# Kernel tuning notes

Measured on AMD Instinct MI355X. Metric: run time of the kernel, lower is better.

Reference implementation:

```python
import jax, jax.numpy as jnp
import numpy as np

QLEN, BSZ, D_MODEL = 1024, 4, 1024
N_HEAD, D_HEAD = 16, 64
RLEN = QLEN  # rlen == klen -> classic _rel_shift path
LN_EPS = 1e-5


def setup_inputs() -> dict:
    key = jax.random.key(0)
    ks = jax.random.split(key, 9)
    s = 0.02
    w = jax.random.normal(ks[0], (QLEN, BSZ, D_MODEL), jnp.float32)
    r = jax.random.normal(ks[1], (RLEN, D_MODEL), jnp.float32)
    # causal mask: True = masked (future positions)
    attn_mask = jnp.triu(jnp.ones((QLEN, QLEN), jnp.bool_), k=1)
    qkv_w = jax.random.normal(ks[2], (D_MODEL, 3 * N_HEAD * D_HEAD), jnp.float32) * s
    r_w = jax.random.normal(ks[3], (D_MODEL, N_HEAD * D_HEAD), jnp.float32) * s
    o_w = jax.random.normal(ks[4], (N_HEAD * D_HEAD, D_MODEL), jnp.float32) * s
    r_r_bias = jax.random.normal(ks[5], (N_HEAD, D_HEAD), jnp.float32) * s
    r_w_bias = jax.random.normal(ks[6], (N_HEAD, D_HEAD), jnp.float32) * s
    ln_g = jnp.ones((D_MODEL,), jnp.float32)
    ln_b = jnp.zeros((D_MODEL,), jnp.float32)
    return {"w": w, "r": r, "attn_mask": attn_mask, "qkv_w": qkv_w,
            "r_w": r_w, "o_w": o_w, "r_r_bias": r_r_bias,
            "r_w_bias": r_w_bias, "ln_g": ln_g, "ln_b": ln_b}


def _rel_shift(x):
    # x: [qlen, klen, bsz, n_head] -> Transformer-XL relative shift
    q, k, b, n = x.shape
    zero_pad = jnp.zeros((q, 1, b, n), x.dtype)
    x_padded = jnp.concatenate([zero_pad, x], axis=1)      # [q, k+1, b, n]
    x_padded = x_padded.reshape(k + 1, q, b, n)
    return x_padded[1:].reshape(q, k, b, n)


def _layer_norm(x, g, b):
    mu = jnp.mean(x, axis=-1, keepdims=True)
    var = jnp.mean(jnp.square(x - mu), axis=-1, keepdims=True)
    return (x - mu) * jax.lax.rsqrt(var + LN_EPS) * g + b


def reference(w, r, attn_mask, qkv_w, r_w, o_w, r_r_bias, r_w_bias, ln_g, ln_b):
    qlen, bsz, _ = w.shape
    H, D = r_r_bias.shape
    scale = 1.0 / D ** 0.5

    w_heads = w @ qkv_w                                    # [q, b, 3*H*D]
    q_h, k_h, v_h = jnp.split(w_heads, 3, axis=-1)
    q_h = q_h.reshape(qlen, bsz, H, D)
    k_h = k_h.reshape(qlen, bsz, H, D)
    v_h = v_h.reshape(qlen, bsz, H, D)
    r_k = (r @ r_w).reshape(-1, H, D)                      # [rlen, H, D]

    AC = jnp.einsum('ibnd,jbnd->ijbn', q_h + r_w_bias, k_h)
    BD = _rel_shift(jnp.einsum('ibnd,jnd->ijbn', q_h + r_r_bias, r_k))
    score = (AC + BD) * scale                              # [q, k, b, n]
    score = jnp.where(attn_mask[:, :, None, None], -1e30, score)

    prob = jax.nn.softmax(score, axis=1)
    vec = jnp.einsum('ijbn,jbnd->ibnd', prob, v_h).reshape(qlen, bsz, H * D)
    attn_out = vec @ o_w
    return _layer_norm(w + attn_out, ln_g, ln_b)
```

## Files before the change

### kernel.cpp

```cpp
#include <hip/hip_runtime.h>
#include <hip/hip_bf16.h>

#define SEQ    1024
#define BSZW   4
#define DMODEL 1024
#define NHEAD  16
#define DHEAD  64
#define MROWS  (SEQ*BSZW)
#define QKVN   (3*NHEAD*DHEAD)

typedef __attribute__((ext_vector_type(8))) short short8;
typedef __attribute__((ext_vector_type(4))) float f32x4;

__device__ __forceinline__ float bf2f(short s) {
    union { int i; float f; } u; u.i = ((int)(unsigned short)s) << 16; return u.f;
}
__device__ __forceinline__ short f2bf(float f) {
    union { float f; unsigned int u; } v; v.f = f;
    unsigned int r = v.u + 0x7FFFu + ((v.u >> 16) & 1u);
    return (short)(unsigned short)(r >> 16);
}

__device__ __forceinline__ void async16(const void* g, void* s) {
    __builtin_amdgcn_global_load_lds(
        (__attribute__((address_space(1))) void*)(g),
        (__attribute__((address_space(3))) void*)(s), 16, 0, 0);
}

__global__ __launch_bounds__(256) void prep_all(const float* __restrict__ w,
                                                const float* __restrict__ r,
                                                const float* __restrict__ qkv_w,
                                                const float* __restrict__ r_w,
                                                const float* __restrict__ o_w,
                                                short* __restrict__ Wb,
                                                short* __restrict__ rb,
                                                short* __restrict__ QKVt,
                                                short* __restrict__ RWt,
                                                short* __restrict__ OWt)
{
    const int z = blockIdx.z;
    const int tid = threadIdx.x;
    if (z == 3) {
        size_t flat = (size_t)blockIdx.y * 96 + blockIdx.x;
        if (flat >= 2560) return;
        size_t idx = flat * 2048 + (size_t)tid * 8;
        const float* in = w; short* out = Wb;
        if (idx >= (size_t)4194304) { in = r; out = rb; idx -= 4194304; }
        float4 a = *(const float4*)(in + idx);
        float4 b = *(const float4*)(in + idx + 4);
        out[idx + 0] = f2bf(a.x); out[idx + 1] = f2bf(a.y);
        out[idx + 2] = f2bf(a.z); out[idx + 3] = f2bf(a.w);
        out[idx + 4] = f2bf(b.x); out[idx + 5] = f2bf(b.y);
        out[idx + 6] = f2bf(b.z); out[idx + 7] = f2bf(b.w);
        return;
    }
    const int bx = blockIdx.x, by = blockIdx.y;
    const float* in; short* out; int C;
    if (z == 0)      { in = qkv_w; out = QKVt; C = QKVN; }
    else if (z == 1) { in = r_w;   out = RWt;  C = DMODEL; if (bx >= 32) return; }
    else             { in = o_w;   out = OWt;  C = DMODEL; if (bx >= 32) return; }
    const int R = DMODEL;
    __shared__ short t[32][33];
    const int rr0 = tid >> 5, c = tid & 31;
    #pragma unroll
    for (int rr = 0; rr < 4; ++rr) {
        int rl = rr0 + rr * 8;
        t[c][rl] = f2bf(in[(size_t)(by * 32 + rl) * C + bx * 32 + c]);
    }
    __syncthreads();
    #pragma unroll
    for (int rr = 0; rr < 4; ++rr) {
        int rl = rr0 + rr * 8;
        out[(size_t)(bx * 32 + rl) * R + by * 32 + c] = t[rl][c];
    }
}

__global__ __launch_bounds__(256) void vtrans(const short* __restrict__ in,
                                              short* __restrict__ out)
{
    __shared__ short t[32][33];
    const int tid = threadIdx.x;
    const int r = tid >> 5, c = tid & 31;
    const int bx = blockIdx.x, by = blockIdx.y, bh = blockIdx.z;
    #pragma unroll
    for (int rr = 0; rr < 4; ++rr) {
        int rl = r + rr * 8;
        t[c][rl] = in[((size_t)bh * SEQ + bx * 32 + rl) * DHEAD + by * 32 + c];
    }
    __syncthreads();
    #pragma unroll
    for (int rr = 0; rr < 4; ++rr) {
        int rl = r + rr * 8;
        out[((size_t)bh * DHEAD + by * 32 + rl) * SEQ + bx * 32 + c] = t[rl][c];
    }
}

#define GEMM_BODY_128(A_, Bt_, K_)                                             \
    __shared__ short As[128 * 32];                                              \
    __shared__ short Bs[128 * 32];                                              \
    const int w = tid >> 6, lane = tid & 63;                                    \
    const int L15 = lane & 15, quad = lane >> 4;                                \
    const int mq = (w & 1) * 64, nq = (w >> 1) * 64;                            \
    f32x4 acc[4][4];                                                            \
    _Pragma("unroll")                                                           \
    for (int i = 0; i < 4; ++i)                                                 \
        _Pragma("unroll")                                                       \
        for (int j = 0; j < 4; ++j) acc[i][j] = (f32x4){0.f, 0.f, 0.f, 0.f};    \
    const int srow  = w * 16 + (lane >> 2);                                     \
    const int schnk = ((lane & 3) ^ (lane >> 4)) * 8;                           \
    const int rpA = (quad ^ (L15 >> 2)) * 8;                                    \
    for (int k0 = 0; k0 < K_; k0 += 32) {                                       \
        __syncthreads();                                                        \
        _Pragma("unroll")                                                       \
        for (int q = 0; q < 2; ++q) {                                           \
            async16(A_ + (size_t)(m0 + q * 64 + srow) * K_ + k0 + schnk,        \
                    &As[(q * 64 + w * 16) * 32]);                               \
            async16(Bt_ + (size_t)(n0 + q * 64 + srow) * K_ + k0 + schnk,       \
                    &Bs[(q * 64 + w * 16) * 32]);                               \
        }                                                                       \
        __syncthreads();                                                        \
        short8 a[4], b[4];                                                      \
        _Pragma("unroll")                                                       \
        for (int rt = 0; rt < 4; ++rt)                                          \
            a[rt] = *(const short8*)&As[(mq + rt * 16 + L15) * 32 + rpA];       \
        _Pragma("unroll")                                                       \
        for (int ct = 0; ct < 4; ++ct)                                          \
            b[ct] = *(const short8*)&Bs[(nq + ct * 16 + L15) * 32 + rpA];       \
        _Pragma("unroll")                                                       \
        for (int rt = 0; rt < 4; ++rt)                                          \
            _Pragma("unroll")                                                   \
            for (int ct = 0; ct < 4; ++ct)                                      \
                acc[rt][ct] = __builtin_amdgcn_mfma_f32_16x16x32_bf16(          \
                    a[rt], b[ct], acc[rt][ct], 0, 0, 0);                        \
    }

__global__ __launch_bounds__(256) void qkv_rk_mfma(const short* __restrict__ Wb,
                                                   const short* __restrict__ QKVt,
                                                   const short* __restrict__ rbuf,
                                                   const short* __restrict__ RWt,
                                                   const float* __restrict__ rwb,
                                                   const float* __restrict__ rrb,
                                                   short* __restrict__ Qwb,
                                                   short* __restrict__ Qrb,
                                                   short* __restrict__ Kb,
                                                   short* __restrict__ Vb,
                                                   short* __restrict__ RK)
{
    const int tid = threadIdx.x;
    const int by = blockIdx.y;
    const bool isrk = (by >= 32);
    if (isrk && blockIdx.x >= 8) return;
    const short* A_  = isrk ? rbuf : Wb;
    const short* Bt_ = isrk ? RWt : QKVt;
    const int m0 = (isrk ? (by - 32) : by) * 128;
    const int n0 = blockIdx.x * 128;
    GEMM_BODY_128(A_, Bt_, 1024)

    if (isrk) {
        const int h = (n0 + nq) >> 6;
        #pragma unroll
        for (int rt = 0; rt < 4; ++rt)
            #pragma unroll
            for (int g = 0; g < 4; ++g) {
                int m = m0 + mq + rt * 16 + quad * 4 + g;
                #pragma unroll
                for (int ct = 0; ct < 4; ++ct)
                    RK[((size_t)h * SEQ + m) * DHEAD + ct * 16 + L15] =
                        f2bf(acc[rt][ct][g]);
            }
        return;
    }
    const int nb = n0 + nq;
    const int chunk = nb >> 10;
    const int h = (nb >> 6) & 15;
    float rw4[4], rr4[4];
    if (chunk == 0) {
        #pragma unroll
        for (int ct = 0; ct < 4; ++ct) {
            rw4[ct] = rwb[h * DHEAD + ct * 16 + L15];
            rr4[ct] = rrb[h * DHEAD + ct * 16 + L15];
        }
    }
    #pragma unroll
    for (int rt = 0; rt < 4; ++rt)
        #pragma unroll
        for (int g = 0; g < 4; ++g) {
            int m = m0 + mq + rt * 16 + quad * 4 + g;
            int qi = m >> 2, b = m & 3;
            size_t rowbase = ((size_t)(b * NHEAD + h) * SEQ + qi) * DHEAD;
            #pragma unroll
            for (int ct = 0; ct < 4; ++ct) {
                int d = ct * 16 + L15;
                float v = acc[rt][ct][g];
                if (chunk == 0) {
                    Qwb[rowbase + d] = f2bf(v + rw4[ct]);
                    Qrb[rowbase + d] = f2bf(v + rr4[ct]);
                } else if (chunk == 1) {
                    Kb[rowbase + d] = f2bf(v);
                } else {
                    Vb[rowbase + d] = f2bf(v);
                }
            }
        }
}

__global__ __launch_bounds__(256) void oproj_mfma(const short* __restrict__ A,
                                                  const short* __restrict__ Bt,
                                                  float* __restrict__ C)
{
    __shared__ short As[128 * 32];
    __shared__ short Bs[64 * 32];
    const int tid = threadIdx.x;
    const int w = tid >> 6, lane = tid & 63;
    const int L15 = lane & 15, quad = lane >> 4;
    const int n0 = blockIdx.x * 64, m0 = blockIdx.y * 128;
    const int mq = w * 32;
    f32x4 acc[2][4];
    #pragma unroll
    for (int i = 0; i < 2; ++i)
        #pragma unroll
        for (int j = 0; j < 4; ++j) acc[i][j] = (f32x4){0.f, 0.f, 0.f, 0.f};
    const int srow  = w * 16 + (lane >> 2);
    const int schnk = ((lane & 3) ^ (lane >> 4)) * 8;
    const int rpA = (quad ^ (L15 >> 2)) * 8;
    for (int k0 = 0; k0 < 1024; k0 += 32) {
        __syncthreads();
        #pragma unroll
        for (int q = 0; q < 2; ++q)
            async16(A + (size_t)(m0 + q * 64 + srow) * 1024 + k0 + schnk,
                    &As[(q * 64 + w * 16) * 32]);
        async16(Bt + (size_t)(n0 + srow) * 1024 + k0 + schnk, &Bs[(w * 16) * 32]);
        __syncthreads();
        short8 a[2], b[4];
        #pragma unroll
        for (int rt = 0; rt < 2; ++rt)
            a[rt] = *(const short8*)&As[(mq + rt * 16 + L15) * 32 + rpA];
        #pragma unroll
        for (int ct = 0; ct < 4; ++ct)
            b[ct] = *(const short8*)&Bs[(ct * 16 + L15) * 32 + rpA];
        #pragma unroll
        for (int rt = 0; rt < 2; ++rt)
            #pragma unroll
            for (int ct = 0; ct < 4; ++ct)
                acc[rt][ct] = __builtin_amdgcn_mfma_f32_16x16x32_bf16(
                    a[rt], b[ct], acc[rt][ct], 0, 0, 0);
    }
    #pragma unroll
    for (int rt = 0; rt < 2; ++rt)
        #pragma unroll
        for (int g = 0; g < 4; ++g) {
            int m = m0 + mq + rt * 16 + quad * 4 + g;
            #pragma unroll
            for (int ct = 0; ct < 4; ++ct)
                C[(size_t)m * DMODEL + n0 + ct * 16 + L15] = acc[rt][ct][g];
        }
}

__global__ __launch_bounds__(256) void attn_mfma(const short* __restrict__ Qw,
                                                 const short* __restrict__ Qr,
                                                 const short* __restrict__ Kg,
                                                 const short* __restrict__ Vt,
                                                 const short* __restrict__ RK,
                                                 short* __restrict__ ATT)
{
    __shared__ short Ks[2][64 * 64];
    __shared__ short Vts[2][64 * 64];
    __shared__ short Pbuf[4][16][136];

    const int tid  = threadIdx.x;
    const int w    = tid >> 6;
    const int lane = tid & 63;
    const int L15  = lane & 15;
    const int quad = lane >> 4;
    const int bh   = blockIdx.x;
    const int it   = 15 - (int)blockIdx.y;
    const int h    = bh & (NHEAD - 1);
    const int b    = bh >> 4;
    const int C    = 63 - 16 * w;

    const short* Kbh = Kg + (size_t)bh * SEQ * DHEAD;
    const short* Vbh = Vt + (size_t)bh * DHEAD * SEQ;
    const short* Rh  = RK + (size_t)h * SEQ * DHEAD;

    const int srow  = w * 8 + (lane >> 3);
    const int schnk = ((lane & 7) ^ (lane >> 3)) * 8;
    const int rp0 = ((quad)     ^ (L15 & 7)) * 8;
    const int rp1 = ((quad + 4) ^ (L15 & 7)) * 8;

    short8 vone;
    #pragma unroll
    for (int i = 0; i < 8; ++i) vone[i] = (short)0x3F80;

    short8 qwf[2], qrf[2];
    {
        const short* qb = Qw + ((size_t)bh * SEQ + it * 64 + w * 16 + L15) * DHEAD + quad * 8;
        qwf[0] = *(const short8*)qb;
        qwf[1] = *(const short8*)(qb + 32);
        const short* qc = Qr + ((size_t)bh * SEQ + it * 64 + w * 16 + L15) * DHEAD + quad * 8;
        qrf[0] = *(const short8*)qc;
        qrf[1] = *(const short8*)(qc + 32);
    }

    f32x4 O[4], Ol;
    #pragma unroll
    for (int c = 0; c < 4; ++c) { O[c] = (f32x4){0.f, 0.f, 0.f, 0.f}; }
    Ol = (f32x4){0.f, 0.f, 0.f, 0.f};

    #pragma unroll
    for (int q = 0; q < 2; ++q) {
        int rr = q * 32 + srow;
        async16(Kbh + (size_t)rr * DHEAD + schnk, &Ks[0][(q * 32 + w * 8) * 64]);
        async16(Vbh + (size_t)rr * SEQ + schnk,   &Vts[0][(q * 32 + w * 8) * 64]);
    }

    for (int jt = 0; jt <= it; ++jt) {
        const int buf = jt & 1;
        const int j0  = jt * 64;
        const int rel0 = 960 + 64 * (jt - it);

        __syncthreads();

        short8 rb0[5], rb1[5];
        #pragma unroll
        for (int cp = 0; cp < 5; ++cp) {
            int ct  = (3 - w) + cp;
            int rel = rel0 + ct * 16 + L15;
            rel = (rel > SEQ - 1) ? (SEQ - 1) : rel;
            const short* rp = Rh + (size_t)rel * DHEAD + quad * 8;
            rb0[cp] = *(const short8*)rp;
            rb1[cp] = *(const short8*)(rp + 32);
        }

        if (jt < it) {
            const int j0n = j0 + 64;
            #pragma unroll
            for (int q = 0; q < 2; ++q) {
                int rr = q * 32 + srow;
                async16(Kbh + (size_t)(j0n + rr) * DHEAD + schnk,
                        &Ks[buf ^ 1][(q * 32 + w * 8) * 64]);
                async16(Vbh + (size_t)rr * SEQ + j0n + schnk,
                        &Vts[buf ^ 1][(q * 32 + w * 8) * 64]);
            }
        }

        f32x4 S[4];
        #pragma unroll
        for (int ct = 0; ct < 4; ++ct) {
            short8 b0 = *(const short8*)&Ks[buf][(ct * 16 + L15) * 64 + rp0];
            short8 b1 = *(const short8*)&Ks[buf][(ct * 16 + L15) * 64 + rp1];
            f32x4 acc = (f32x4){0.f, 0.f, 0.f, 0.f};
            acc = __builtin_amdgcn_mfma_f32_16x16x32_bf16(qwf[0], b0, acc, 0, 0, 0);
            acc = __builtin_amdgcn_mfma_f32_16x16x32_bf16(qwf[1], b1, acc, 0, 0, 0);
            S[ct] = acc;
        }

        #pragma unroll
        for (int cp = 0; cp < 5; ++cp) {
            int ct = (3 - w) + cp;
            f32x4 p = (f32x4){0.f, 0.f, 0.f, 0.f};
            p = __builtin_amdgcn_mfma_f32_16x16x32_bf16(qrf[0], rb0[cp], p, 0, 0, 0);
            p = __builtin_amdgcn_mfma_f32_16x16x32_bf16(qrf[1], rb1[cp], p, 0, 0, 0);
            #pragma unroll
            for (int g = 0; g < 4; ++g)
                Pbuf[w][quad * 4 + g][ct * 16 + L15] = f2bf(p[g]);
        }

        #pragma unroll
        for (int ct = 0; ct < 4; ++ct) {
            #pragma unroll
            for (int g = 0; g < 4; ++g) {
                int r = quad * 4 + g;
                int t = ct * 16 + L15 - r + C;
                float bd = bf2f(Pbuf[w][r][t]);
                S[ct][g] = (S[ct][g] + bd) * 0.125f;
            }
        }
        if (jt == it) {
            #pragma unroll
            for (int ct = 0; ct < 4; ++ct)
                #pragma unroll
                for (int g = 0; g < 4; ++g) {
                    int i = it * 64 + w * 16 + quad * 4 + g;
                    int j = j0 + ct * 16 + L15;
                    if (j > i) S[ct][g] = -1e30f;
                }
        }

        #pragma unroll
        for (int ct = 0; ct < 4; ++ct)
            #pragma unroll
            for (int g = 0; g < 4; ++g)
                Pbuf[w][quad * 4 + g][ct * 16 + L15] =
                    f2bf(__expf(S[ct][g] - 20.0f));
        short8 pa0 = *(const short8*)&Pbuf[w][L15][quad * 8];
        short8 pa1 = *(const short8*)&Pbuf[w][L15][32 + quad * 8];

        #pragma unroll
        for (int ct = 0; ct < 4; ++ct) {
            short8 v0 = *(const short8*)&Vts[buf][(ct * 16 + L15) * 64 + rp0];
            short8 v1 = *(const short8*)&Vts[buf][(ct * 16 + L15) * 64 + rp1];
            O[ct] = __builtin_amdgcn_mfma_f32_16x16x32_bf16(pa0, v0, O[ct], 0, 0, 0);
            O[ct] = __builtin_amdgcn_mfma_f32_16x16x32_bf16(pa1, v1, O[ct], 0, 0, 0);
        }
        Ol = __builtin_amdgcn_mfma_f32_16x16x32_bf16(pa0, vone, Ol, 0, 0, 0);
        Ol = __builtin_amdgcn_mfma_f32_16x16x32_bf16(pa1, vone, Ol, 0, 0, 0);
    }

    #pragma unroll
    for (int g = 0; g < 4; ++g) {
        float inv = 1.0f / Ol[g];
        int i = it * 64 + w * 16 + quad * 4 + g;
        #pragma unroll
        for (int ct = 0; ct < 4; ++ct)
            ATT[((size_t)i * BSZW + b) * DMODEL + h * DHEAD + ct * 16 + L15] =
                f2bf(O[ct][g] * inv);
    }
}

__global__ __launch_bounds__(256) void ln_kernel(const float* __restrict__ w,
                                                 const float* __restrict__ AO,
                                                 const float* __restrict__ g,
                                                 const float* __restrict__ bb,
                                                 float* __restrict__ out)
{
    __shared__ float red[256];
    __shared__ float sh_mu, sh_rs;
    const int m = blockIdx.x;
    const int tid = threadIdx.x;
    const int j0 = tid * 4;
    float4 xw = *(const float4*)(w + (size_t)m * DMODEL + j0);
    float4 xa = *(const float4*)(AO + (size_t)m * DMODEL + j0);
    float x[4] = {xw.x + xa.x, xw.y + xa.y, xw.z + xa.z, xw.w + xa.w};
    red[tid] = x[0] + x[1] + x[2] + x[3];
    __syncthreads();
    for (int st = 128; st > 0; st >>= 1) {
        if (tid < st) red[tid] += red[tid + st];
        __syncthreads();
    }
    if (tid == 0) sh_mu = red[0] * (1.0f / DMODEL);
    __syncthreads();
    const float mu = sh_mu;
    float v = 0.0f;
    #pragma unroll
    for (int k = 0; k < 4; ++k) { float d = x[k] - mu; v += d * d; }
    red[tid] = v;
    __syncthreads();
    for (int st = 128; st > 0; st >>= 1) {
        if (tid < st) red[tid] += red[tid + st];
        __syncthreads();
    }
    if (tid == 0) sh_rs = rsqrtf(red[0] * (1.0f / DMODEL) + 1e-5f);
    __syncthreads();
    const float rs = sh_rs;
    float4 g4 = *(const float4*)(g + j0);
    float4 b4 = *(const float4*)(bb + j0);
    float4 o4;
    o4.x = (x[0] - mu) * rs * g4.x + b4.x;
    o4.y = (x[1] - mu) * rs * g4.y + b4.y;
    o4.z = (x[2] - mu) * rs * g4.z + b4.z;
    o4.w = (x[3] - mu) * rs * g4.w + b4.w;
    *(float4*)(out + (size_t)m * DMODEL + j0) = o4;
}

extern "C" void kernel_launch(void* const* d_in, const int* in_sizes, int n_in,
                              void* d_out, int out_size, void* d_ws, size_t ws_size,
                              hipStream_t stream)
{
    (void)in_sizes; (void)n_in; (void)out_size; (void)ws_size;
    const float* w     = (const float*)d_in[0];
    const float* r     = (const float*)d_in[1];
    const float* qkv_w = (const float*)d_in[3];
    const float* r_w   = (const float*)d_in[4];
    const float* o_w   = (const float*)d_in[5];
    const float* rrb   = (const float*)d_in[6];
    const float* rwb   = (const float*)d_in[7];
    const float* ln_g  = (const float*)d_in[8];
    const float* ln_b  = (const float*)d_in[9];
    float* out = (float*)d_out;

    const size_t M1 = 1024 * 1024;
    short* Wb   = (short*)d_ws;
    short* QKVt = Wb   + 4 * M1;
    short* rb   = QKVt + 3 * M1;
    short* RWt  = rb   + 1 * M1;
    short* OWt  = RWt  + 1 * M1;
    short* Qwb  = OWt  + 1 * M1;
    short* Qrb  = Qwb  + 4 * M1;
    short* Kb   = Qrb  + 4 * M1;
    short* Vb   = Kb   + 4 * M1;
    short* Vtb  = Vb   + 4 * M1;
    short* RKb  = Vtb  + 4 * M1;
    short* ATTb = Vb;
    float* AO   = (float*)d_ws;

    prep_all<<<dim3(QKVN / 32, DMODEL / 32, 4), 256, 0, stream>>>(
        w, r, qkv_w, r_w, o_w, Wb, rb, QKVt, RWt, OWt);

    qkv_rk_mfma<<<dim3(QKVN / 128, 40), 256, 0, stream>>>(Wb, QKVt, rb, RWt,
                                                          rwb, rrb,
                                                          Qwb, Qrb, Kb, Vb, RKb);
    vtrans<<<dim3(SEQ / 32, DHEAD / 32, BSZW * NHEAD), 256, 0, stream>>>(Vb, Vtb);
    attn_mfma<<<dim3(BSZW * NHEAD, 16), 256, 0, stream>>>(Qwb, Qrb, Kb, Vtb, RKb, ATTb);
    oproj_mfma<<<dim3(DMODEL / 64, MROWS / 128), 256, 0, stream>>>(ATTb, OWt, AO);
    ln_kernel<<<MROWS, 256, 0, stream>>>(w, AO, ln_g, ln_b, out);
}
```

Before: 242.8 us.

## Double-buffer LDS tiles in QKV and output-projection GEMMs, compact r_k grid

Both MFMA GEMM kernels now use two LDS buffers. The next K-tile's async global-to-LDS loads are issued right after the barrier, so they overlap the MFMA work on the current tile, and one of the two barriers per iteration is removed. The r_k projection blocks are packed into 3 extra grid rows instead of 8, which cuts the number of blocks that launch only to exit. In exchange, LDS use per block doubles, which may lower occupancy, and correctness depends on the barrier waiting for the outstanding async loads.

```diff
diff --git a/kernel.cpp b/kernel.cpp
--- a/kernel.cpp
+++ b/kernel.cpp
@@ -95,9 +95,9 @@
     }
 }
 
-#define GEMM_BODY_128(A_, Bt_, K_)                                             \
-    __shared__ short As[128 * 32];                                              \
-    __shared__ short Bs[128 * 32];                                              \
+#define GEMM_BODY_128_DB(A_, Bt_, K_)                                           \
+    __shared__ short As[2][128 * 32];                                           \
+    __shared__ short Bs[2][128 * 32];                                           \
     const int w = tid >> 6, lane = tid & 63;                                    \
     const int L15 = lane & 15, quad = lane >> 4;                                \
     const int mq = (w & 1) * 64, nq = (w >> 1) * 64;                            \
@@ -109,23 +109,32 @@
     const int srow  = w * 16 + (lane >> 2);                                     \
     const int schnk = ((lane & 3) ^ (lane >> 4)) * 8;                           \
     const int rpA = (quad ^ (L15 >> 2)) * 8;                                    \
+    _Pragma("unroll")                                                           \
+    for (int q = 0; q < 2; ++q) {                                               \
+        async16(A_ + (size_t)(m0 + q * 64 + srow) * K_ + schnk,                 \
+                &As[0][(q * 64 + w * 16) * 32]);                                \
+        async16(Bt_ + (size_t)(n0 + q * 64 + srow) * K_ + schnk,                \
+                &Bs[0][(q * 64 + w * 16) * 32]);                                \
+    }                                                                           \
     for (int k0 = 0; k0 < K_; k0 += 32) {                                       \
-        __syncthreads();                                                        \
-        _Pragma("unroll")                                                       \
-        for (int q = 0; q < 2; ++q) {                                           \
-            async16(A_ + (size_t)(m0 + q * 64 + srow) * K_ + k0 + schnk,        \
-                    &As[(q * 64 + w * 16) * 32]);                               \
-            async16(Bt_ + (size_t)(n0 + q * 64 + srow) * K_ + k0 + schnk,       \
-                    &Bs[(q * 64 + w * 16) * 32]);                               \
+        const int bu = (k0 >> 5) & 1;                                           \
+        __syncthreads();                                  \
+        if (k0 + 32 < K_) {                                                     \
+            _Pragma("unroll")                                                   \
+            for (int q = 0; q < 2; ++q) {                                       \
+                async16(A_ + (size_t)(m0 + q * 64 + srow) * K_ + k0 + 32 + schnk, \
+                        &As[bu ^ 1][(q * 64 + w * 16) * 32]);                   \
+                async16(Bt_ + (size_t)(n0 + q * 64 + srow) * K_ + k0 + 32 + schnk, \
+                        &Bs[bu ^ 1][(q * 64 + w * 16) * 32]);                   \
+            }                                                                   \
         }                                                                       \
-        __syncthreads();                                                        \
         short8 a[4], b[4];                                                      \
         _Pragma("unroll")                                                       \
         for (int rt = 0; rt < 4; ++rt)                                          \
-            a[rt] = *(const short8*)&As[(mq + rt * 16 + L15) * 32 + rpA];       \
+            a[rt] = *(const short8*)&As[bu][(mq + rt * 16 + L15) * 32 + rpA];   \
         _Pragma("unroll")                                                       \
         for (int ct = 0; ct < 4; ++ct)                                          \
-            b[ct] = *(const short8*)&Bs[(nq + ct * 16 + L15) * 32 + rpA];       \
+            b[ct] = *(const short8*)&Bs[bu][(nq + ct * 16 + L15) * 32 + rpA];   \
         _Pragma("unroll")                                                       \
         for (int rt = 0; rt < 4; ++rt)                                          \
             _Pragma("unroll")                                                   \
@@ -149,12 +158,19 @@
     const int tid = threadIdx.x;
     const int by = blockIdx.y;
     const bool isrk = (by >= 32);
-    if (isrk && blockIdx.x >= 8) return;
+    int m0, n0;
+    if (isrk) {
+        int t = (by - 32) * 24 + blockIdx.x;
+        if (t >= 64) return;
+        m0 = (t >> 3) * 128;
+        n0 = (t & 7) * 128;
+    } else {
+        m0 = by * 128;
+        n0 = blockIdx.x * 128;
+    }
     const short* A_  = isrk ? rbuf : Wb;
     const short* Bt_ = isrk ? RWt : QKVt;
-    const int m0 = (isrk ? (by - 32) : by) * 128;
-    const int n0 = blockIdx.x * 128;
-    GEMM_BODY_128(A_, Bt_, 1024)
+    GEMM_BODY_128_DB(A_, Bt_, 1024)
 
     if (isrk) {
         const int h = (n0 + nq) >> 6;
@@ -208,8 +224,8 @@
                                                   const short* __restrict__ Bt,
                                                   float* __restrict__ C)
 {
-    __shared__ short As[128 * 32];
-    __shared__ short Bs[64 * 32];
+    __shared__ short As[2][128 * 32];
+    __shared__ short Bs[2][64 * 32];
     const int tid = threadIdx.x;
     const int w = tid >> 6, lane = tid & 63;
     const int L15 = lane & 15, quad = lane >> 4;
@@ -223,21 +239,29 @@
     const int srow  = w * 16 + (lane >> 2);
     const int schnk = ((lane & 3) ^ (lane >> 4)) * 8;
     const int rpA = (quad ^ (L15 >> 2)) * 8;
+    #pragma unroll
+    for (int q = 0; q < 2; ++q)
+        async16(A + (size_t)(m0 + q * 64 + srow) * 1024 + schnk,
+                &As[0][(q * 64 + w * 16) * 32]);
+    async16(Bt + (size_t)(n0 + srow) * 1024 + schnk, &Bs[0][(w * 16) * 32]);
     for (int k0 = 0; k0 < 1024; k0 += 32) {
+        const int bu = (k0 >> 5) & 1;
         __syncthreads();
-        #pragma unroll
-        for (int q = 0; q < 2; ++q)
-            async16(A + (size_t)(m0 + q * 64 + srow) * 1024 + k0 + schnk,
-                    &As[(q * 64 + w * 16) * 32]);
-        async16(Bt + (size_t)(n0 + srow) * 1024 + k0 + schnk, &Bs[(w * 16) * 32]);
-        __syncthreads();
+        if (k0 + 32 < 1024) {
+            #pragma unroll
+            for (int q = 0; q < 2; ++q)
+                async16(A + (size_t)(m0 + q * 64 + srow) * 1024 + k0 + 32 + schnk,
+                        &As[bu ^ 1][(q * 64 + w * 16) * 32]);
+            async16(Bt + (size_t)(n0 + srow) * 1024 + k0 + 32 + schnk,
+                    &Bs[bu ^ 1][(w * 16) * 32]);
+        }
         short8 a[2], b[4];
         #pragma unroll
         for (int rt = 0; rt < 2; ++rt)
-            a[rt] = *(const short8*)&As[(mq + rt * 16 + L15) * 32 + rpA];
+            a[rt] = *(const short8*)&As[bu][(mq + rt * 16 + L15) * 32 + rpA];
         #pragma unroll
         for (int ct = 0; ct < 4; ++ct)
-            b[ct] = *(const short8*)&Bs[(ct * 16 + L15) * 32 + rpA];
+            b[ct] = *(const short8*)&Bs[bu][(ct * 16 + L15) * 32 + rpA];
         #pragma unroll
         for (int rt = 0; rt < 2; ++rt)
             #pragma unroll
@@ -496,7 +520,7 @@
     prep_all<<<dim3(QKVN / 32, DMODEL / 32, 4), 256, 0, stream>>>(
         w, r, qkv_w, r_w, o_w, Wb, rb, QKVt, RWt, OWt);
 
-    qkv_rk_mfma<<<dim3(QKVN / 128, 40), 256, 0, stream>>>(Wb, QKVt, rb, RWt,
+    qkv_rk_mfma<<<dim3(QKVN / 128, 35), 256, 0, stream>>>(Wb, QKVt, rb, RWt,
                                                           rwb, rrb,
                                                           Qwb, Qrb, Kb, Vb, RKb);
     vtrans<<<dim3(SEQ / 32, DHEAD / 32, BSZW * NHEAD), 256, 0, stream>>>(Vb, Vtb);
```

Result: slower. 250.8 us (+3.3%).
